# Optimization experiments

Measured on AMD Instinct MI355X. Metric: run time of the kernel, lower is better.

The kernel has to match this reference:

```python
import jax, jax.numpy as jnp
import numpy as np
from jax.scipy.special import erf

N, M = 2048, 32


def setup_inputs() -> dict:
    key = jax.random.key(0)
    k1, k2, k3, k4 = jax.random.split(key, 4)
    predicted_risk = jax.random.normal(k1, (N, M), dtype=jnp.float32)
    expressions = jax.random.normal(k2, (N, M), dtype=jnp.float32)
    predicted_tr = jax.random.normal(k3, (N, M), dtype=jnp.float32)
    event_indicator = (jax.random.uniform(k4, (N, M)) < 0.3).astype(jnp.float32)
    sigma = jnp.float32(1.0)
    return {
        "predicted_risk": predicted_risk,
        "expressions": expressions,
        "predicted_tr": predicted_tr,
        "event_indicator": event_indicator,
        "sigma": sigma,
    }


def reference(predicted_risk, expressions, predicted_tr, event_indicator, sigma):
    # time_indicator: (n, m), normalized per-feature and scaled by 2*sigma*sqrt(2)
    ti = jnp.exp(expressions - predicted_tr)
    ti = ti / jnp.max(ti, axis=0) / (2.0 * sigma * jnp.sqrt(jnp.float32(2.0)))
    n, m = expressions.shape
    # location[j, a, k] = ti[j, k] - ti[a, k]   -> (n, n, m)
    location = ti[:, None, :] - ti[None, :, :]
    phi = 0.5 * (1.0 + erf(-location))
    # diagonal correction: phi[i, i, :] += 0.5
    idx = jnp.arange(n)
    phi = phi.at[idx, idx].add(0.5)
    # cumsum^T[j, k] = sum_a exp(predicted_risk[a, k]) * phi[j, a, k]
    expH = jnp.exp(predicted_risk)  # (n, m)
    log_cumsum = jnp.log(jnp.einsum('am,jam->jm', expH, phi))  # (n, m)
    sum_loglik = jnp.sum((predicted_risk - log_cumsum) * event_indicator)
    return -sum_loglik
```

## Files before the change

### kernel.cpp

```cpp
#include <hip/hip_runtime.h>
#include <math.h>

#define NROWS 2048
#define MCOLS 32

#define C1 1.1283791671f
#define C3 (-0.3761263890f)
#define C5 0.1128379167f
#define C7 (-0.0268661706f)

__global__ __launch_bounds__(256) void k_init(float* __restrict__ Mp,
                                              unsigned int* __restrict__ maxbits,
                                              float* __restrict__ out) {
    int t = threadIdx.x;
    Mp[t] = 0.0f;
    if (t < MCOLS) maxbits[t] = 0u;
    if (t == 0) out[0] = 0.0f;
}

__global__ __launch_bounds__(256) void k_elem(const float* __restrict__ expr,
                                              const float* __restrict__ tr,
                                              const float* __restrict__ risk,
                                              float* __restrict__ ws_t,
                                              float* __restrict__ ws_e,
                                              float* __restrict__ Mp,
                                              unsigned int* __restrict__ maxbits) {
    int tid = threadIdx.x;
    int i = blockIdx.x * 256 + tid;
    float tv = __expf(expr[i] - tr[i]);
    float ev = __expf(risk[i]);
    ws_t[i] = tv;
    ws_e[i] = ev;

    __shared__ float sm_t[256];
    __shared__ float sm_e[256];
    sm_t[tid] = tv; sm_e[tid] = ev;
    __syncthreads();

    int k = tid & 31;
    int q = tid >> 5;
    float partial = 0.0f, mx = 0.0f;
#pragma unroll
    for (int r = 0; r < 8; r++) {
        float t = sm_t[r * 32 + k];
        float e = sm_e[r * 32 + k];
        float p = e;
        for (int m = 0; m < q; m++) p *= t;
        partial += p;
        mx = fmaxf(mx, t);
    }
    atomicAdd(&Mp[q * 32 + k], partial);
    if (q == 0) atomicMax(&maxbits[k], __float_as_uint(mx));
}

__global__ __launch_bounds__(64) void k_coeff(const float* __restrict__ Mp,
                                              const unsigned int* __restrict__ maxbits,
                                              const float* __restrict__ sigma,
                                              float* __restrict__ D,
                                              float* __restrict__ scaleS,
                                              float* __restrict__ Shalf) {
    int k = threadIdx.x;
    if (k >= MCOLS) return;
    float s = 1.0f / (__uint_as_float(maxbits[k]) * 2.0f * sigma[0] * sqrtf(2.0f));
    float M[8];
    float sp = 1.0f;
#pragma unroll
    for (int q = 0; q < 8; q++) { M[q] = Mp[q * 32 + k] * sp; sp *= s; }
    D[0 * 32 + k] = C1 * M[1] +         C3 * M[3] +         C5 * M[5] +        C7 * M[7];
    D[1 * 32 + k] = C1 * M[0] + 3.0f *  C3 * M[2] + 5.0f *  C5 * M[4] + 7.0f * C7 * M[6];
    D[2 * 32 + k] = 3.0f * C3 * M[1] + 10.0f * C5 * M[3] + 21.0f * C7 * M[5];
    D[3 * 32 + k] = C3 * M[0] + 10.0f * C5 * M[2] + 35.0f * C7 * M[4];
    D[4 * 32 + k] = 5.0f * C5 * M[1] + 35.0f * C7 * M[3];
    D[5 * 32 + k] = C5 * M[0] + 21.0f * C7 * M[2];
    D[6 * 32 + k] = 7.0f * C7 * M[1];
    D[7 * 32 + k] = C7 * M[0];
    scaleS[k] = s;
    Shalf[k]  = 0.5f * M[0];
}

__global__ __launch_bounds__(256) void k_final(const float* __restrict__ ws_t,
                                               const float* __restrict__ ws_e,
                                               const float* __restrict__ D,
                                               const float* __restrict__ scaleS,
                                               const float* __restrict__ Shalf,
                                               const float* __restrict__ risk,
                                               const float* __restrict__ event,
                                               float* __restrict__ out) {
    int tid = threadIdx.x;
    int i = blockIdx.x * 256 + tid;
    __shared__ float sD[256];
    __shared__ float sSc[32];
    __shared__ float sSh[32];
    __shared__ float warpsum[4];
    sD[tid] = D[tid];
    if (tid < 32) { sSc[tid] = scaleS[tid]; sSh[tid] = Shalf[tid]; }
    __syncthreads();

    int k = i & 31;
    float w = -(ws_t[i] * sSc[k]);
    float acc = sD[7 * 32 + k];
#pragma unroll
    for (int q = 6; q >= 0; q--)
        acc = fmaf(acc, w, sD[q * 32 + k]);
    float cum = sSh[k] + 0.5f * (acc + ws_e[i]);
    float c = (__logf(cum) - risk[i]) * event[i];

    for (int off = 32; off > 0; off >>= 1)
        c += __shfl_down(c, off, 64);
    if ((tid & 63) == 0) warpsum[tid >> 6] = c;
    __syncthreads();
    if (tid == 0) {
        float s = (warpsum[0] + warpsum[1]) + (warpsum[2] + warpsum[3]);
        atomicAdd(out, s);
    }
}

extern "C" void kernel_launch(void* const* d_in, const int* in_sizes, int n_in,
                              void* d_out, int out_size, void* d_ws, size_t ws_size,
                              hipStream_t stream) {
    const float* risk  = (const float*)d_in[0];
    const float* expr  = (const float*)d_in[1];
    const float* tr    = (const float*)d_in[2];
    const float* event = (const float*)d_in[3];
    const float* sigma = (const float*)d_in[4];
    float* out = (float*)d_out;

    float*        ws_t    = (float*)d_ws;
    float*        ws_e    = ws_t + NROWS * MCOLS;
    float*        ws_Mp   = ws_e + NROWS * MCOLS;
    float*        ws_D    = ws_Mp + 8 * MCOLS;
    float*        ws_sc   = ws_D + 8 * MCOLS;
    float*        ws_Sh   = ws_sc + MCOLS;
    unsigned int* ws_max  = (unsigned int*)(ws_Sh + MCOLS);

    k_init<<<1, 256, 0, stream>>>(ws_Mp, ws_max, out);
    k_elem<<<(NROWS * MCOLS) / 256, 256, 0, stream>>>(expr, tr, risk, ws_t, ws_e,
                                                      ws_Mp, ws_max);
    k_coeff<<<1, 64, 0, stream>>>(ws_Mp, ws_max, sigma, ws_D, ws_sc, ws_Sh);
    k_final<<<(NROWS * MCOLS) / 256, 256, 0, stream>>>(ws_t, ws_e, ws_D, ws_sc,
                                                       ws_Sh, risk, event, out);
}
```

Before: 76.84 us.

## Fuse four launches into one cooperative kernel with grid-wide sync

Replaces the init, elementwise, coefficient and final kernels with a single cooperative kernel of 64 blocks. Each block handles 4 tiles and keeps the exp values in registers, so the workspace round-trip for t and e is gone. Per-block moment and max partials replace global atomics, and every block reduces them redundantly after a grid.sync. This removes several launch and inter-kernel gaps, in exchange for cooperative-launch overhead and a grid barrier with lower parallelism.

```diff
diff --git a/kernel.cpp b/kernel.cpp
--- a/kernel.cpp
+++ b/kernel.cpp
@@ -1,118 +1,130 @@
 #include <hip/hip_runtime.h>
+#include <hip/hip_cooperative_groups.h>
 #include <math.h>
+
+namespace cg = cooperative_groups;
 
 #define NROWS 2048
 #define MCOLS 32
+#define NBLK  64
+#define TPB   256
+#define ELEMS 4
 
 #define C1 1.1283791671f
 #define C3 (-0.3761263890f)
 #define C5 0.1128379167f
 #define C7 (-0.0268661706f)
 
-__global__ __launch_bounds__(256) void k_init(float* __restrict__ Mp,
-                                              unsigned int* __restrict__ maxbits,
-                                              float* __restrict__ out) {
-    int t = threadIdx.x;
-    Mp[t] = 0.0f;
-    if (t < MCOLS) maxbits[t] = 0u;
-    if (t == 0) out[0] = 0.0f;
-}
+__global__ __launch_bounds__(TPB) void k_fused(const float* __restrict__ risk,
+                                               const float* __restrict__ expr,
+                                               const float* __restrict__ tr,
+                                               const float* __restrict__ event,
+                                               const float* __restrict__ sigma,
+                                               float* __restrict__ partM,
+                                               float* __restrict__ partMax,
+                                               float* __restrict__ out) {
+    cg::grid_group grid = cg::this_grid();
+    const int tid = threadIdx.x;
+    const int bid = blockIdx.x;
+    const int k = tid & 31;
+    const int q = tid >> 5;
 
-__global__ __launch_bounds__(256) void k_elem(const float* __restrict__ expr,
-                                              const float* __restrict__ tr,
-                                              const float* __restrict__ risk,
-                                              float* __restrict__ ws_t,
-                                              float* __restrict__ ws_e,
-                                              float* __restrict__ Mp,
-                                              unsigned int* __restrict__ maxbits) {
-    int tid = threadIdx.x;
-    int i = blockIdx.x * 256 + tid;
-    float tv = __expf(expr[i] - tr[i]);
-    float ev = __expf(risk[i]);
-    ws_t[i] = tv;
-    ws_e[i] = ev;
+    if (bid == 0 && tid == 0) out[0] = 0.0f;
 
-    __shared__ float sm_t[256];
-    __shared__ float sm_e[256];
-    sm_t[tid] = tv; sm_e[tid] = ev;
+    __shared__ float sm_t[TPB];
+    __shared__ float sm_e[TPB];
+
+    float tv[ELEMS], ev[ELEMS], rk[ELEMS];
+    float partial = 0.0f, mx = 0.0f;
+
+#pragma unroll
+    for (int r = 0; r < ELEMS; r++) {
+        const int i = (bid * ELEMS + r) * TPB + tid;
+        const float rv = risk[i];
+        tv[r] = __expf(expr[i] - tr[i]);
+        ev[r] = __expf(rv);
+        rk[r] = rv;
+
+        sm_t[tid] = tv[r];
+        sm_e[tid] = ev[r];
+        __syncthreads();
+#pragma unroll
+        for (int row = 0; row < 8; row++) {
+            const float t = sm_t[row * 32 + k];
+            const float e = sm_e[row * 32 + k];
+            float p = e;
+            for (int m = 0; m < q; m++) p *= t;
+            partial += p;
+            mx = fmaxf(mx, t);
+        }
+        __syncthreads();
+    }
+    partM[bid * 256 + tid] = partial;
+    if (q == 0) partMax[bid * 32 + k] = mx;
+
+    grid.sync();
+
+    __shared__ float sM[256];
+    __shared__ float sMax[32];
+    {
+        float msum = 0.0f;
+#pragma unroll
+        for (int b = 0; b < NBLK; b++) msum += partM[b * 256 + tid];
+        sM[tid] = msum;
+        if (q == 0) {
+            float m2 = 0.0f;
+#pragma unroll
+            for (int b = 0; b < NBLK; b++) m2 = fmaxf(m2, partMax[b * 32 + k]);
+            sMax[k] = m2;
+        }
+    }
     __syncthreads();
 
-    int k = tid & 31;
-    int q = tid >> 5;
-    float partial = 0.0f, mx = 0.0f;
-#pragma unroll
-    for (int r = 0; r < 8; r++) {
-        float t = sm_t[r * 32 + k];
-        float e = sm_e[r * 32 + k];
-        float p = e;
-        for (int m = 0; m < q; m++) p *= t;
-        partial += p;
-        mx = fmaxf(mx, t);
-    }
-    atomicAdd(&Mp[q * 32 + k], partial);
-    if (q == 0) atomicMax(&maxbits[k], __float_as_uint(mx));
-}
-
-__global__ __launch_bounds__(64) void k_coeff(const float* __restrict__ Mp,
-                                              const unsigned int* __restrict__ maxbits,
-                                              const float* __restrict__ sigma,
-                                              float* __restrict__ D,
-                                              float* __restrict__ scaleS,
-                                              float* __restrict__ Shalf) {
-    int k = threadIdx.x;
-    if (k >= MCOLS) return;
-    float s = 1.0f / (__uint_as_float(maxbits[k]) * 2.0f * sigma[0] * sqrtf(2.0f));
-    float M[8];
-    float sp = 1.0f;
-#pragma unroll
-    for (int q = 0; q < 8; q++) { M[q] = Mp[q * 32 + k] * sp; sp *= s; }
-    D[0 * 32 + k] = C1 * M[1] +         C3 * M[3] +         C5 * M[5] +        C7 * M[7];
-    D[1 * 32 + k] = C1 * M[0] + 3.0f *  C3 * M[2] + 5.0f *  C5 * M[4] + 7.0f * C7 * M[6];
-    D[2 * 32 + k] = 3.0f * C3 * M[1] + 10.0f * C5 * M[3] + 21.0f * C7 * M[5];
-    D[3 * 32 + k] = C3 * M[0] + 10.0f * C5 * M[2] + 35.0f * C7 * M[4];
-    D[4 * 32 + k] = 5.0f * C5 * M[1] + 35.0f * C7 * M[3];
-    D[5 * 32 + k] = C5 * M[0] + 21.0f * C7 * M[2];
-    D[6 * 32 + k] = 7.0f * C7 * M[1];
-    D[7 * 32 + k] = C7 * M[0];
-    scaleS[k] = s;
-    Shalf[k]  = 0.5f * M[0];
-}
-
-__global__ __launch_bounds__(256) void k_final(const float* __restrict__ ws_t,
-                                               const float* __restrict__ ws_e,
-                                               const float* __restrict__ D,
-                                               const float* __restrict__ scaleS,
-                                               const float* __restrict__ Shalf,
-                                               const float* __restrict__ risk,
-                                               const float* __restrict__ event,
-                                               float* __restrict__ out) {
-    int tid = threadIdx.x;
-    int i = blockIdx.x * 256 + tid;
     __shared__ float sD[256];
     __shared__ float sSc[32];
     __shared__ float sSh[32];
-    __shared__ float warpsum[4];
-    sD[tid] = D[tid];
-    if (tid < 32) { sSc[tid] = scaleS[tid]; sSh[tid] = Shalf[tid]; }
+    {
+        const float s = 1.0f / (sMax[k] * 2.0f * sigma[0] * sqrtf(2.0f));
+        float M[8];
+        float sp = 1.0f;
+#pragma unroll
+        for (int j = 0; j < 8; j++) { M[j] = sM[j * 32 + k] * sp; sp *= s; }
+        float d;
+        if      (q == 0) d = C1 * M[1] +         C3 * M[3] +         C5 * M[5] +        C7 * M[7];
+        else if (q == 1) d = C1 * M[0] + 3.0f *  C3 * M[2] + 5.0f *  C5 * M[4] + 7.0f * C7 * M[6];
+        else if (q == 2) d = 3.0f * C3 * M[1] + 10.0f * C5 * M[3] + 21.0f * C7 * M[5];
+        else if (q == 3) d = C3 * M[0] + 10.0f * C5 * M[2] + 35.0f * C7 * M[4];
+        else if (q == 4) d = 5.0f * C5 * M[1] + 35.0f * C7 * M[3];
+        else if (q == 5) d = C5 * M[0] + 21.0f * C7 * M[2];
+        else if (q == 6) d = 7.0f * C7 * M[1];
+        else             d = C7 * M[0];
+        sD[tid] = d;
+        if (q == 0) { sSc[k] = s; sSh[k] = 0.5f * M[0]; }
+    }
     __syncthreads();
 
-    int k = i & 31;
-    float w = -(ws_t[i] * sSc[k]);
-    float acc = sD[7 * 32 + k];
+    float csum = 0.0f;
+    const float sck = sSc[k];
+    const float shk = sSh[k];
 #pragma unroll
-    for (int q = 6; q >= 0; q--)
-        acc = fmaf(acc, w, sD[q * 32 + k]);
-    float cum = sSh[k] + 0.5f * (acc + ws_e[i]);
-    float c = (__logf(cum) - risk[i]) * event[i];
+    for (int r = 0; r < ELEMS; r++) {
+        const int i = (bid * ELEMS + r) * TPB + tid;
+        const float w = -(tv[r] * sck);
+        float acc = sD[7 * 32 + k];
+#pragma unroll
+        for (int p = 6; p >= 0; p--)
+            acc = fmaf(acc, w, sD[p * 32 + k]);
+        const float cum = shk + 0.5f * (acc + ev[r]);
+        csum += (__logf(cum) - rk[r]) * event[i];
+    }
 
     for (int off = 32; off > 0; off >>= 1)
-        c += __shfl_down(c, off, 64);
-    if ((tid & 63) == 0) warpsum[tid >> 6] = c;
+        csum += __shfl_down(csum, off, 64);
+    __shared__ float wsum[4];
+    if ((tid & 63) == 0) wsum[tid >> 6] = csum;
     __syncthreads();
-    if (tid == 0) {
-        float s = (warpsum[0] + warpsum[1]) + (warpsum[2] + warpsum[3]);
-        atomicAdd(out, s);
-    }
+    if (tid == 0)
+        atomicAdd(out, (wsum[0] + wsum[1]) + (wsum[2] + wsum[3]));
 }
 
 extern "C" void kernel_launch(void* const* d_in, const int* in_sizes, int n_in,
@@ -125,18 +137,11 @@
     const float* sigma = (const float*)d_in[4];
     float* out = (float*)d_out;
 
-    float*        ws_t    = (float*)d_ws;
-    float*        ws_e    = ws_t + NROWS * MCOLS;
-    float*        ws_Mp   = ws_e + NROWS * MCOLS;
-    float*        ws_D    = ws_Mp + 8 * MCOLS;
-    float*        ws_sc   = ws_D + 8 * MCOLS;
-    float*        ws_Sh   = ws_sc + MCOLS;
-    unsigned int* ws_max  = (unsigned int*)(ws_Sh + MCOLS);
+    float* partM   = (float*)d_ws;
+    float* partMax = partM + NBLK * 256;
 
-    k_init<<<1, 256, 0, stream>>>(ws_Mp, ws_max, out);
-    k_elem<<<(NROWS * MCOLS) / 256, 256, 0, stream>>>(expr, tr, risk, ws_t, ws_e,
-                                                      ws_Mp, ws_max);
-    k_coeff<<<1, 64, 0, stream>>>(ws_Mp, ws_max, sigma, ws_D, ws_sc, ws_Sh);
-    k_final<<<(NROWS * MCOLS) / 256, 256, 0, stream>>>(ws_t, ws_e, ws_D, ws_sc,
-                                                       ws_Sh, risk, event, out);
+    void* args[] = {(void*)&risk, (void*)&expr, (void*)&tr, (void*)&event,
+                    (void*)&sigma, (void*)&partM, (void*)&partMax, (void*)&out};
+    hipLaunchCooperativeKernel((const void*)k_fused, dim3(NBLK), dim3(TPB),
+                               args, 0, stream);
 }
```

Result: slower. 104.9 us (+36.5%).
